# Kernel optimization log

Hardware: AMD Instinct MI355X
Metric: run time of the kernel (lower is better)

The kernel has to match this reference:

```python
import jax, jax.numpy as jnp
import numpy as np

SEL = [46, 92]
NEURON = [24, 48, 96]
AXIS = 8
NNEI = sum(SEL)            # 138
NDESCRPT = NNEI * 4        # 552
NFRAMES = 32
NATOMS0 = 192
N = NFRAMES * NATOMS0      # 6144 atom rows


def setup_inputs() -> dict:
    key = jax.random.key(0)
    ks = jax.random.split(key, 25)
    inp = {"dmatrix": jax.random.normal(ks[0], (N, NDESCRPT), dtype=jnp.float32)}
    dims = [1] + NEURON
    i = 1
    for t in range(len(SEL)):
        for l in range(len(NEURON)):
            nin, nout = dims[l], dims[l + 1]
            inp[f"w{t}_{l}"] = (jax.random.normal(ks[i], (nin, nout), dtype=jnp.float32)
                                 / np.float32(np.sqrt(nin + nout)))
            i += 1
            inp[f"b{t}_{l}"] = jax.random.normal(ks[i], (1, nout), dtype=jnp.float32)
            i += 1
    inp["nframes"] = NFRAMES
    return inp


def _type_mlp(x, Ws, bs):
    # x: [M, 1] radial channel; ResidualLinear chain 1->24->48->96.
    h = jnp.tanh(x @ Ws[0] + bs[0])                       # 1->24: no residual
    for l in (1, 2):                                      # doubling residual paths
        hn = jnp.tanh(h @ Ws[l] + bs[l])
        h = jnp.concatenate([h, h], axis=-1) + hn
    return h                                              # [M, 96]


def reference(dmatrix, w0_0, b0_0, w0_1, b0_1, w0_2, b0_2,
              w1_0, b1_0, w1_1, b1_1, w1_2, b1_2, nframes):
    params = [((w0_0, w0_1, w0_2), (b0_0, b0_1, b0_2)),
              ((w1_0, w1_1, w1_2), (b1_0, b1_1, b1_2))]
    M = NEURON[-1]
    acc = 0.0
    off = 0
    for t, (Ws, bs) in enumerate(params):
        sel = SEL[t]
        # per-type neighbor slice: [N, sel, 4]
        dd = dmatrix[:, off * 4:(off + sel) * 4].reshape(-1, sel, 4)
        g = _type_mlp(dd[:, :, 0:1].reshape(-1, 1), Ws, bs).reshape(-1, sel, M)
        # [N,4,sel] @ [N,sel,96] -> [N,4,96]
        acc = acc + jnp.einsum('nsd,nse->nde', dd, g)
        off += sel
    xs = acc / np.float32(NNEI)                           # [N, 4, 96]
    # [N,96,4] @ [N,4,axis] -> [N,96,axis]
    res = jnp.einsum('nde,ndk->nek', xs, xs[:, :, :AXIS])
    return res.reshape(nframes, -1)                       # [nframes, natoms0*96*axis]
```

## Files before the change

### kernel.cpp

```cpp
#include <hip/hip_runtime.h>
#include <hip/hip_fp16.h>

typedef _Float16 f16;

__global__ __launch_bounds__(128)
void build_table(const float* __restrict__ w00, const float* __restrict__ b00,
                 const float* __restrict__ w01, const float* __restrict__ b01,
                 const float* __restrict__ w02, const float* __restrict__ b02,
                 const float* __restrict__ w10, const float* __restrict__ b10,
                 const float* __restrict__ w11, const float* __restrict__ b11,
                 const float* __restrict__ w12, const float* __restrict__ b12,
                 f16* __restrict__ tab, int nseg, float xmin, float h)
{
    __shared__ float h0s[24];
    __shared__ float h1s[48];

    const int row  = blockIdx.x;
    const int rows = nseg + 1;
    const int ty   = (row >= rows) ? 1 : 0;
    const int i    = ty ? (row - rows) : row;
    const float x  = __builtin_fmaf((float)i, h, xmin);
    const int tid  = threadIdx.x;

    const float* __restrict__ W0 = ty ? w10 : w00;
    const float* __restrict__ B0 = ty ? b10 : b00;
    const float* __restrict__ W1 = ty ? w11 : w01;
    const float* __restrict__ B1 = ty ? b11 : b01;
    const float* __restrict__ W2 = ty ? w12 : w02;
    const float* __restrict__ B2 = ty ? b12 : b02;

    if (tid < 24)
        h0s[tid] = tanhf(__builtin_fmaf(x, W0[tid], B0[tid]));
    __syncthreads();

    if (tid < 48) {
        float a = B1[tid];
#pragma unroll
        for (int j = 0; j < 24; ++j)
            a = __builtin_fmaf(h0s[j], W1[j * 48 + tid], a);
        h1s[tid] = tanhf(a) + h0s[(tid < 24) ? tid : (tid - 24)];
    }
    __syncthreads();

    if (tid < 96) {
        float a = B2[tid];
#pragma unroll
        for (int k = 0; k < 48; ++k)
            a = __builtin_fmaf(h1s[k], W2[k * 96 + tid], a);
        tab[(size_t)row * 96 + tid] = (f16)(tanhf(a) + h1s[(tid < 48) ? tid : (tid - 48)]);
    }
}

__global__ __launch_bounds__(192, 4)
void emb_main(const float* __restrict__ dmat, const f16* __restrict__ tab,
              int nseg, float scale, float offs,
              float* __restrict__ out)
{
    __shared__ float DD[144 * 4];
    __shared__ float Y2s[3 * 4 * 96];

    const int tid = threadIdx.x, n = blockIdx.x;
    const int w = tid >> 6, lane = tid & 63;
    const int l15 = lane & 15, lhi = lane >> 4;

    if (lane < 48) {
        const int t = w + 3 * (lane >> 4);
        const int r = t * 16 + (lane & 15);
        const bool t0 = (t < 3);
        const int  s  = t0 ? r : (r - 2);
        const bool ok = t0 ? (r < 46) : (r < 140);
        float4 v = make_float4(0.f, 0.f, 0.f, 0.f);
        if (ok) v = *reinterpret_cast<const float4*>(dmat + (size_t)n * 552 + s * 4);
        *reinterpret_cast<float4*>(&DD[r * 4]) = v;
    }

    float yp[24];
#pragma unroll
    for (int i = 0; i < 24; ++i) yp[i] = 0.f;

    const float clampHi = (float)nseg - 0.5f;
    const int rowU32 = 48;

    for (int t = w; t < 9; t += 3) {
        const int tyt = (t >= 3);
        const uint32_t* __restrict__ tb =
            reinterpret_cast<const uint32_t*>(tab + (size_t)tyt * (nseg + 1) * 96);

        int irow[4]; float fr[4]; float4 dd4[4];
#pragma unroll
        for (int rg = 0; rg < 4; ++rg) {
            const int r = t * 16 + lhi * 4 + rg;
            const float x = DD[r * 4];
            float u = __builtin_fmaf(x, scale, offs);
            u = fminf(fmaxf(u, 0.f), clampHi);
            const int i = (int)u;
            irow[rg] = i * rowU32;
            fr[rg]   = u - (float)i;
            dd4[rg]  = *reinterpret_cast<const float4*>(&DD[r * 4]);
        }

#pragma unroll
        for (int c = 0; c < 3; ++c) {
#pragma unroll
            for (int rg = 0; rg < 4; ++rg) {
                const uint32_t* p = tb + irow[rg] + c * 16 + l15;
                const uint32_t alo = p[0];
                const uint32_t ahi = p[rowU32];
                const __half2 lo2 = *reinterpret_cast<const __half2*>(&alo);
                const __half2 hi2 = *reinterpret_cast<const __half2*>(&ahi);
                const float2 lo = __half22float2(lo2);
                const float2 hi = __half22float2(hi2);
                const float g0 = __builtin_fmaf(fr[rg], hi.x - lo.x, lo.x);
                const float g1 = __builtin_fmaf(fr[rg], hi.y - lo.y, lo.y);
                const int b = c * 8;
                yp[b + 0] = __builtin_fmaf(dd4[rg].x, g0, yp[b + 0]);
                yp[b + 1] = __builtin_fmaf(dd4[rg].y, g0, yp[b + 1]);
                yp[b + 2] = __builtin_fmaf(dd4[rg].z, g0, yp[b + 2]);
                yp[b + 3] = __builtin_fmaf(dd4[rg].w, g0, yp[b + 3]);
                yp[b + 4] = __builtin_fmaf(dd4[rg].x, g1, yp[b + 4]);
                yp[b + 5] = __builtin_fmaf(dd4[rg].y, g1, yp[b + 5]);
                yp[b + 6] = __builtin_fmaf(dd4[rg].z, g1, yp[b + 6]);
                yp[b + 7] = __builtin_fmaf(dd4[rg].w, g1, yp[b + 7]);
            }
        }
    }

#pragma unroll
    for (int i = 0; i < 24; ++i) {
        float v = yp[i];
        v += __shfl_xor(v, 16);
        v += __shfl_xor(v, 32);
        yp[i] = v;
    }
    if (lhi == 0) {
#pragma unroll
        for (int c = 0; c < 3; ++c)
#pragma unroll
            for (int d = 0; d < 4; ++d) {
                const float2 v2 = make_float2(yp[c * 8 + d], yp[c * 8 + 4 + d]);
                *reinterpret_cast<float2*>(&Y2s[w * 384 + d * 96 + c * 32 + 2 * l15]) = v2;
            }
    }
    __syncthreads();

    if (tid < 96) {
        constexpr float inv = 1.0f / 138.0f;
        const float x0 = (Y2s[tid]       + Y2s[384 + tid]       + Y2s[768 + tid])       * inv;
        const float x1 = (Y2s[96 + tid]  + Y2s[384 + 96 + tid]  + Y2s[768 + 96 + tid])  * inv;
        const float x2 = (Y2s[192 + tid] + Y2s[384 + 192 + tid] + Y2s[768 + 192 + tid]) * inv;
        const float x3 = (Y2s[288 + tid] + Y2s[384 + 288 + tid] + Y2s[768 + 288 + tid]) * inv;
        float rv[8];
#pragma unroll
        for (int k = 0; k < 8; ++k) {
            const float k0 = (Y2s[k]       + Y2s[384 + k]       + Y2s[768 + k])       * inv;
            const float k1 = (Y2s[96 + k]  + Y2s[384 + 96 + k]  + Y2s[768 + 96 + k])  * inv;
            const float k2 = (Y2s[192 + k] + Y2s[384 + 192 + k] + Y2s[768 + 192 + k]) * inv;
            const float k3 = (Y2s[288 + k] + Y2s[384 + 288 + k] + Y2s[768 + 288 + k]) * inv;
            float rr = x0 * k0;
            rr = __builtin_fmaf(x1, k1, rr);
            rr = __builtin_fmaf(x2, k2, rr);
            rr = __builtin_fmaf(x3, k3, rr);
            rv[k] = rr;
        }
        float* op = out + (size_t)n * 768 + tid * 8;
        *reinterpret_cast<float4*>(op)     = make_float4(rv[0], rv[1], rv[2], rv[3]);
        *reinterpret_cast<float4*>(op + 4) = make_float4(rv[4], rv[5], rv[6], rv[7]);
    }
}

extern "C" void kernel_launch(void* const* d_in, const int* in_sizes, int n_in,
                              void* d_out, int out_size, void* d_ws, size_t ws_size,
                              hipStream_t stream)
{
    const float* dmat = (const float*)d_in[0];
    const int n_atoms = in_sizes[0] / 552;

    int nseg = 2048;
    while ((size_t)2 * (size_t)(nseg + 1) * 96 * sizeof(f16) > ws_size && nseg > 16)
        nseg >>= 1;
    const float xmin = -8.f, xmax = 8.f;
    const float h     = (xmax - xmin) / (float)nseg;
    const float scale = (float)nseg / (xmax - xmin);
    const float offs  = -xmin * scale;
    f16* tab = (f16*)d_ws;

    const int rows2 = 2 * (nseg + 1);
    build_table<<<rows2, 128, 0, stream>>>(
        (const float*)d_in[1],  (const float*)d_in[2],
        (const float*)d_in[3],  (const float*)d_in[4],
        (const float*)d_in[5],  (const float*)d_in[6],
        (const float*)d_in[7],  (const float*)d_in[8],
        (const float*)d_in[9],  (const float*)d_in[10],
        (const float*)d_in[11], (const float*)d_in[12],
        tab, nseg, xmin, h);

    emb_main<<<n_atoms, 192, 0, stream>>>(dmat, tab, nseg, scale, offs, (float*)d_out);
}
```

Measured before the change: 40.97 us.

## Batch eight table rows per block and halve lookup table resolution

The table-building kernel now computes eight interpolation rows per block. Each thread caches its weight column in registers and reuses it across those rows, so weights are no longer reloaded for every row and fewer, fuller blocks are launched. The table resolution also drops from 2048 to 1024 segments. That halves the table-build work and shrinks the table footprint for the main kernel's gathers, at the cost of coarser linear interpolation accuracy.

```diff
diff --git a/kernel.cpp b/kernel.cpp
--- a/kernel.cpp
+++ b/kernel.cpp
@@ -10,17 +10,14 @@
                  const float* __restrict__ w10, const float* __restrict__ b10,
                  const float* __restrict__ w11, const float* __restrict__ b11,
                  const float* __restrict__ w12, const float* __restrict__ b12,
-                 f16* __restrict__ tab, int nseg, float xmin, float h)
+                 f16* __restrict__ tab, int rowsPerType, float xmin, float h)
 {
-    __shared__ float h0s[24];
-    __shared__ float h1s[48];
-
-    const int row  = blockIdx.x;
-    const int rows = nseg + 1;
-    const int ty   = (row >= rows) ? 1 : 0;
-    const int i    = ty ? (row - rows) : row;
-    const float x  = __builtin_fmaf((float)i, h, xmin);
-    const int tid  = threadIdx.x;
+    __shared__ float h0s[8][24];
+    __shared__ float h1s[8][48];
+
+    const int ty  = blockIdx.y;
+    const int r0  = blockIdx.x * 8;
+    const int tid = threadIdx.x;
 
     const float* __restrict__ W0 = ty ? w10 : w00;
     const float* __restrict__ B0 = ty ? b10 : b00;
@@ -29,25 +26,53 @@
     const float* __restrict__ W2 = ty ? w12 : w02;
     const float* __restrict__ B2 = ty ? b12 : b02;
 
-    if (tid < 24)
-        h0s[tid] = tanhf(__builtin_fmaf(x, W0[tid], B0[tid]));
+#pragma unroll
+    for (int p = 0; p < 2; ++p) {
+        const int idx = p * 128 + tid;
+        if (idx < 192) {
+            const int q = idx / 24, j = idx - q * 24;
+            const float x = __builtin_fmaf((float)(r0 + q), h, xmin);
+            h0s[q][j] = tanhf(__builtin_fmaf(x, W0[j], B0[j]));
+        }
+    }
     __syncthreads();
 
-    if (tid < 48) {
-        float a = B1[tid];
-#pragma unroll
-        for (int j = 0; j < 24; ++j)
-            a = __builtin_fmaf(h0s[j], W1[j * 48 + tid], a);
-        h1s[tid] = tanhf(a) + h0s[(tid < 24) ? tid : (tid - 24)];
+    if (tid < 96) {
+        const int half = tid / 48, k = tid - half * 48;
+        float w1c[24];
+#pragma unroll
+        for (int j = 0; j < 24; ++j) w1c[j] = W1[j * 48 + k];
+        const float bk = B1[k];
+        const int km = (k < 24) ? k : (k - 24);
+#pragma unroll
+        for (int qq = 0; qq < 4; ++qq) {
+            const int q = half * 4 + qq;
+            float a = bk;
+#pragma unroll
+            for (int j = 0; j < 24; ++j)
+                a = __builtin_fmaf(h0s[q][j], w1c[j], a);
+            h1s[q][k] = tanhf(a) + h0s[q][km];
+        }
     }
     __syncthreads();
 
     if (tid < 96) {
-        float a = B2[tid];
-#pragma unroll
-        for (int k = 0; k < 48; ++k)
-            a = __builtin_fmaf(h1s[k], W2[k * 96 + tid], a);
-        tab[(size_t)row * 96 + tid] = (f16)(tanhf(a) + h1s[(tid < 48) ? tid : (tid - 48)]);
+        const int e = tid;
+        float w2c[48];
+#pragma unroll
+        for (int k = 0; k < 48; ++k) w2c[k] = W2[k * 96 + e];
+        const float be = B2[e];
+        const int em = (e < 48) ? e : (e - 48);
+#pragma unroll
+        for (int q = 0; q < 8; ++q) {
+            if (r0 + q < rowsPerType) {
+                float a = be;
+#pragma unroll
+                for (int k = 0; k < 48; ++k)
+                    a = __builtin_fmaf(h1s[q][k], w2c[k], a);
+                tab[((size_t)ty * rowsPerType + r0 + q) * 96 + e] = (f16)(tanhf(a) + h1s[q][em]);
+            }
+        }
     }
 }
 
@@ -175,7 +200,7 @@
     const float* dmat = (const float*)d_in[0];
     const int n_atoms = in_sizes[0] / 552;
 
-    int nseg = 2048;
+    int nseg = 1024;
     while ((size_t)2 * (size_t)(nseg + 1) * 96 * sizeof(f16) > ws_size && nseg > 16)
         nseg >>= 1;
     const float xmin = -8.f, xmax = 8.f;
@@ -184,15 +209,16 @@
     const float offs  = -xmin * scale;
     f16* tab = (f16*)d_ws;
 
-    const int rows2 = 2 * (nseg + 1);
-    build_table<<<rows2, 128, 0, stream>>>(
+    const int rowsPerType = nseg + 1;
+    dim3 bgrid((rowsPerType + 7) / 8, 2);
+    build_table<<<bgrid, 128, 0, stream>>>(
         (const float*)d_in[1],  (const float*)d_in[2],
         (const float*)d_in[3],  (const float*)d_in[4],
         (const float*)d_in[5],  (const float*)d_in[6],
         (const float*)d_in[7],  (const float*)d_in[8],
         (const float*)d_in[9],  (const float*)d_in[10],
         (const float*)d_in[11], (const float*)d_in[12],
-        tab, nseg, xmin, h);
+        tab, rowsPerType, xmin, h);
 
     emb_main<<<n_atoms, 192, 0, stream>>>(dmat, tab, nseg, scale, offs, (float*)d_out);
 }
```

Result: no change. 40.39 us (-1.4%).
